# Kernel tuning notes

Measured on AMD Instinct MI355X. Metric: run time of the kernel, lower is better.

The kernel has to match this reference:

```python
import jax, jax.numpy as jnp
import numpy as np

B, DX, DH, DA, T = 2048, 64, 128, 128, 256
W_SCALE = 0.05


def setup_inputs() -> dict:
    key = jax.random.key(0)
    ks = iter(jax.random.split(key, 64))

    def nrm(shape, s=1.0):
        return jax.random.normal(next(ks), shape, dtype=jnp.float32) * s

    inp = {
        "x_t": nrm((B, DX)),
        "prev_h": nrm((B, DH)),
        "prev_c": nrm((B, DH)),
        "dt": jax.random.uniform(next(ks), (B, 1), dtype=jnp.float32),
        "store": nrm((B, T, DH)),
    }
    # six gates: (x-proj, h-proj, s-proj (or dt for gate s), bias)
    inp.update({
        "W_sx": nrm((DX, DH), W_SCALE), "W_sh": nrm((DH, DH), W_SCALE), "w_st": nrm((1, DH), W_SCALE), "b_s": jnp.zeros((DH,), jnp.float32),
        "W_fx": nrm((DX, DH), W_SCALE), "W_fh": nrm((DH, DH), W_SCALE), "W_fs": nrm((DH, DH), W_SCALE), "b_f": jnp.zeros((DH,), jnp.float32),
        "W_ix": nrm((DX, DH), W_SCALE), "W_ih": nrm((DH, DH), W_SCALE), "W_is": nrm((DH, DH), W_SCALE), "b_i": jnp.zeros((DH,), jnp.float32),
        "W_Tx": nrm((DX, DH), W_SCALE), "W_Th": nrm((DH, DH), W_SCALE), "W_Ts": nrm((DH, DH), W_SCALE), "b_T": jnp.zeros((DH,), jnp.float32),
        "W_ex": nrm((DX, DH), W_SCALE), "W_eh": nrm((DH, DH), W_SCALE), "W_es": nrm((DH, DH), W_SCALE), "b_e": jnp.zeros((DH,), jnp.float32),
        "W_ox": nrm((DX, DH), W_SCALE), "W_oh": nrm((DH, DH), W_SCALE), "W_os": nrm((DH, DH), W_SCALE), "b_o": jnp.zeros((DH,), jnp.float32),
        # additive attention over store: query from (h, new_c), keys from store
        "W_aq": nrm((DH, DA), W_SCALE), "W_ak": nrm((DH, DA), W_SCALE), "W_ah": nrm((DH, DA), W_SCALE),
        "b_a": jnp.zeros((DA,), jnp.float32), "v_a": nrm((DA,), W_SCALE),
        # interaction module: gated blend of h and attention context, gate from x_t
        "W_hh": nrm((DH, DH), W_SCALE), "W_he": nrm((DH, DH), W_SCALE), "W_hg": nrm((DX, DH), W_SCALE), "b_h": jnp.zeros((DH,), jnp.float32),
    })
    return inp


def reference(x_t, prev_h, prev_c, dt, store,
              W_sx, W_sh, w_st, b_s,
              W_fx, W_fh, W_fs, b_f,
              W_ix, W_ih, W_is, b_i,
              W_Tx, W_Th, W_Ts, b_T,
              W_ex, W_eh, W_es, b_e,
              W_ox, W_oh, W_os, b_o,
              W_aq, W_ak, W_ah, b_a, v_a,
              W_hh, W_he, W_hg, b_h):
    # time-aware gate s: dt is a scalar time-delta feature, broadcast over DH
    s = jnp.tanh(prev_h @ W_sh + x_t @ W_sx + dt @ w_st + b_s)            # [B, DH]
    f = jax.nn.sigmoid(prev_h @ W_fh + x_t @ W_fx + s @ W_fs + b_f)
    i = jax.nn.sigmoid(prev_h @ W_ih + x_t @ W_ix + s @ W_is + b_i)
    Tg = jax.nn.sigmoid(prev_h @ W_Th + x_t @ W_Tx + s @ W_Ts + b_T)
    elp = jnp.tanh(prev_h @ W_eh + x_t @ W_ex + s @ W_es + b_e)
    new_c = f * prev_c + i * elp + Tg * s                                  # [B, DH]
    o = jax.nn.sigmoid(prev_h @ W_oh + x_t @ W_ox + s @ W_os + b_o)
    h = o * jax.nn.sigmoid(new_c)                                          # [B, DH]

    # additive attention over the memory `store` [B, T, DH]
    q = h @ W_aq + new_c @ W_ak                                            # [B, DA]
    keys = jnp.einsum('btd,da->bta', store, W_ah)                          # [B, T, DA]
    e = jnp.einsum('bta,a->bt', jnp.tanh(q[:, None, :] + keys + b_a), v_a)  # [B, T]
    alpha = jax.nn.softmax(e, axis=-1)
    ctx = jnp.einsum('bt,btd->bd', alpha, store)                           # [B, DH]

    # interaction module: gated fusion of h and attention context
    g = jax.nn.sigmoid(x_t @ W_hg)
    new_h = g * jnp.tanh(h @ W_hh + ctx @ W_he + b_h)                      # [B, DH]
    return new_c, new_h
```

## Files before the change

kernel.cpp:

```cpp
#include <hip/hip_runtime.h>
#include <hip/hip_bf16.h>

#define B  2048
#define DX 64
#define DH 128
#define DA 128
#define T  256

typedef __attribute__((ext_vector_type(8))) short bf16x8;
typedef __attribute__((ext_vector_type(4))) float f32x4;

__device__ inline unsigned short bfbits(float f) {
    unsigned int u = __float_as_uint(f);
    unsigned int r = (u + 0x7fffu + ((u >> 16) & 1u)) >> 16;
    return (unsigned short)r;
}

__device__ inline float fast_tanh(float x) {
    x = fminf(15.f, fmaxf(-15.f, x));
    float e = __expf(2.f * x);
    return 1.f - 2.f * __builtin_amdgcn_rcpf(e + 1.f);
}

__device__ inline float sigm(float x) {
    return __builtin_amdgcn_rcpf(1.f + __expf(-x));
}

__global__ void k0_wt(const float* __restrict__ Wah, unsigned short* __restrict__ wT) {
    int i = blockIdx.x * 256 + threadIdx.x;
    int d = i >> 7;
    int a = i & 127;
    wT[a * DH + d] = bfbits(Wah[i]);
}

__global__ __launch_bounds__(512) void k1_gates(
    const float* __restrict__ xx,  const float* __restrict__ ph,
    const float* __restrict__ pcv, const float* __restrict__ dtv,
    const float* __restrict__ Wsx, const float* __restrict__ Wsh, const float* __restrict__ wst, const float* __restrict__ bs,
    const float* __restrict__ Wfx, const float* __restrict__ Wfh, const float* __restrict__ Wfs, const float* __restrict__ bf_,
    const float* __restrict__ Wix, const float* __restrict__ Wih, const float* __restrict__ Wis, const float* __restrict__ bi_,
    const float* __restrict__ WTx, const float* __restrict__ WTh, const float* __restrict__ WTs, const float* __restrict__ bT_,
    const float* __restrict__ Wex, const float* __restrict__ Weh, const float* __restrict__ Wes, const float* __restrict__ be_,
    const float* __restrict__ Wox, const float* __restrict__ Woh, const float* __restrict__ Wos, const float* __restrict__ bo_,
    const float* __restrict__ Waq, const float* __restrict__ Wak, const float* __restrict__ Whg,
    float* __restrict__ outc, float* __restrict__ wsh, float* __restrict__ wsq, float* __restrict__ wsg)
{
    __shared__ float shh[8][DH], shx[8][DX], shs[8][DH], shc[8][DH], shn[8][DH];
    const int tid = threadIdx.x;
    const int c   = tid & 127;
    const int qd  = tid >> 7;
    const int r0  = blockIdx.x * 8;
    const int ra  = qd * 2, rb = qd * 2 + 1;

    for (int i = tid; i < 8 * DH; i += 512) shh[i >> 7][i & 127] = ph[(size_t)r0 * DH + i];
    for (int i = tid; i < 8 * DX; i += 512) shx[i >> 6][i & 63]  = xx[(size_t)r0 * DX + i];
    __syncthreads();

    float A0, A1;
    {
        float bb = bs[c], w0 = wst[c];
        A0 = bb + dtv[r0 + ra] * w0;
        A1 = bb + dtv[r0 + rb] * w0;
        for (int k = 0; k < DH; ++k) { float wv = Wsh[k * DH + c]; A0 += shh[ra][k] * wv; A1 += shh[rb][k] * wv; }
        for (int k = 0; k < DX; ++k) { float wv = Wsx[k * DH + c]; A0 += shx[ra][k] * wv; A1 += shx[rb][k] * wv; }
        shs[ra][c] = fast_tanh(A0);
        shs[rb][c] = fast_tanh(A1);
    }
    __syncthreads();

#define G3(Wh_, Wx_, Ws_, b_)                                                              \
    { float bb = (b_)[c]; A0 = bb; A1 = bb;                                                \
      for (int k = 0; k < DH; ++k) { float wv = (Wh_)[k * DH + c];                         \
          A0 += shh[ra][k] * wv; A1 += shh[rb][k] * wv; }                                  \
      for (int k = 0; k < DX; ++k) { float wv = (Wx_)[k * DH + c];                         \
          A0 += shx[ra][k] * wv; A1 += shx[rb][k] * wv; }                                  \
      for (int k = 0; k < DH; ++k) { float wv = (Ws_)[k * DH + c];                         \
          A0 += shs[ra][k] * wv; A1 += shs[rb][k] * wv; } }

    G3(Wfh, Wfx, Wfs, bf_); float f0 = sigm(A0), f1 = sigm(A1);
    G3(Wih, Wix, Wis, bi_); float i0 = sigm(A0), i1 = sigm(A1);
    G3(WTh, WTx, WTs, bT_); float t0 = sigm(A0), t1 = sigm(A1);
    G3(Weh, Wex, Wes, be_); float e0 = fast_tanh(A0), e1 = fast_tanh(A1);
    G3(Woh, Wox, Wos, bo_); float o0 = sigm(A0), o1 = sigm(A1);
#undef G3

    {
        float s0 = shs[ra][c], s1 = shs[rb][c];
        float c0 = f0 * pcv[(size_t)(r0 + ra) * DH + c] + i0 * e0 + t0 * s0;
        float c1 = f1 * pcv[(size_t)(r0 + rb) * DH + c] + i1 * e1 + t1 * s1;
        float h0 = o0 * sigm(c0);
        float h1 = o1 * sigm(c1);
        outc[(size_t)(r0 + ra) * DH + c] = c0;
        outc[(size_t)(r0 + rb) * DH + c] = c1;
        wsh[(size_t)(r0 + ra) * DH + c] = h0;
        wsh[(size_t)(r0 + rb) * DH + c] = h1;
        shc[ra][c] = c0; shc[rb][c] = c1;
        shn[ra][c] = h0; shn[rb][c] = h1;
    }
    {
        A0 = 0.f; A1 = 0.f;
        for (int k = 0; k < DX; ++k) { float wv = Whg[k * DH + c]; A0 += shx[ra][k] * wv; A1 += shx[rb][k] * wv; }
        wsg[(size_t)(r0 + ra) * DH + c] = sigm(A0);
        wsg[(size_t)(r0 + rb) * DH + c] = sigm(A1);
    }
    __syncthreads();
    {
        A0 = 0.f; A1 = 0.f;
        for (int k = 0; k < DH; ++k) {
            float wq_ = Waq[k * DH + c], wk_ = Wak[k * DH + c];
            A0 += shn[ra][k] * wq_ + shc[ra][k] * wk_;
            A1 += shn[rb][k] * wq_ + shc[rb][k] * wk_;
        }
        wsq[(size_t)(r0 + ra) * DH + c] = A0;
        wsq[(size_t)(r0 + rb) * DH + c] = A1;
    }
}

__global__ __launch_bounds__(256, 2) void k2_attn(
    const float* __restrict__ store_, const unsigned short* __restrict__ wt,
    const float* __restrict__ ba, const float* __restrict__ va,
    const float* __restrict__ wsq, float* __restrict__ wsctx)
{
    __shared__ __align__(16) unsigned short ldsA[64][136];
    __shared__ float qb[DA], vv[DA], ee[T], red[8], ctxh[2][DH];

    const int tid = threadIdx.x;
    const int r   = blockIdx.x;
    const int l   = tid & 63;
    const int w   = tid >> 6;
    const int lr  = l & 15;
    const int kg  = l >> 4;
    const float* srow = store_ + (size_t)r * (T * DH);

    if (tid < DA) {
        qb[tid] = wsq[(size_t)r * DA + tid] + ba[tid];
        vv[tid] = va[tid];
    }

    bf16x8 bfr[8][4];
#pragma unroll
    for (int ct = 0; ct < 8; ++ct)
#pragma unroll
        for (int ks = 0; ks < 4; ++ks)
            bfr[ct][ks] = *(const bf16x8*)&wt[(ct * 16 + lr) * DH + ks * 32 + kg * 8];

    for (int tt = 0; tt < 4; ++tt) {
        __syncthreads();
#pragma unroll
        for (int ci = 0; ci < 4; ++ci) {
            int cid = tid + ci * 256;
            int row = cid >> 4;
            int c8  = cid & 15;
            const float* g = srow + ((tt * 64 + row) * DH + c8 * 8);
            float4 u0 = *(const float4*)g;
            float4 u1 = *(const float4*)(g + 4);
            union { unsigned short us[8]; uint4 v; } pk;
            pk.us[0] = bfbits(u0.x); pk.us[1] = bfbits(u0.y);
            pk.us[2] = bfbits(u0.z); pk.us[3] = bfbits(u0.w);
            pk.us[4] = bfbits(u1.x); pk.us[5] = bfbits(u1.y);
            pk.us[6] = bfbits(u1.z); pk.us[7] = bfbits(u1.w);
            *(uint4*)&ldsA[row][c8 * 8] = pk.v;
        }
        __syncthreads();

        f32x4 acc[8];
#pragma unroll
        for (int ct = 0; ct < 8; ++ct) acc[ct] = (f32x4){0.f, 0.f, 0.f, 0.f};
        const int arow = w * 16 + lr;
#pragma unroll
        for (int ks = 0; ks < 4; ++ks) {
            bf16x8 af = *(const bf16x8*)&ldsA[arow][ks * 32 + kg * 8];
#pragma unroll
            for (int ct = 0; ct < 8; ++ct)
                acc[ct] = __builtin_amdgcn_mfma_f32_16x16x32_bf16(af, bfr[ct][ks], acc[ct], 0, 0, 0);
        }

        float pe[4] = {0.f, 0.f, 0.f, 0.f};
#pragma unroll
        for (int ct = 0; ct < 8; ++ct) {
            int a = ct * 16 + lr;
            float qa = qb[a], vva = vv[a];
#pragma unroll
            for (int reg = 0; reg < 4; ++reg)
                pe[reg] += vva * fast_tanh(qa + acc[ct][reg]);
        }
#pragma unroll
        for (int m = 1; m <= 8; m <<= 1) {
#pragma unroll
            for (int reg = 0; reg < 4; ++reg) pe[reg] += __shfl_xor(pe[reg], m);
        }
        if (lr == 0) {
#pragma unroll
            for (int reg = 0; reg < 4; ++reg)
                ee[tt * 64 + w * 16 + kg * 4 + reg] = pe[reg];
        }
    }
    __syncthreads();

    float xv = ee[tid];
    float mx = xv;
#pragma unroll
    for (int m = 1; m < 64; m <<= 1) mx = fmaxf(mx, __shfl_xor(mx, m));
    if (l == 0) red[w] = mx;
    __syncthreads();
    float M = fmaxf(fmaxf(red[0], red[1]), fmaxf(red[2], red[3]));
    float ex = __expf(xv - M);
    float sm = ex;
#pragma unroll
    for (int m = 1; m < 64; m <<= 1) sm += __shfl_xor(sm, m);
    if (l == 0) red[4 + w] = sm;
    __syncthreads();
    float S = red[4] + red[5] + red[6] + red[7];
    ee[tid] = ex / S;
    __syncthreads();

    {
        int d = tid & 127, th = tid >> 7;
        const float* sp = srow + (size_t)th * 128 * DH + d;
        float p = 0.f;
        for (int t = 0; t < 128; ++t) p = fmaf(ee[th * 128 + t], sp[(size_t)t * DH], p);
        ctxh[th][d] = p;
    }
    __syncthreads();
    if (tid < DH) wsctx[(size_t)r * DH + tid] = ctxh[0][tid] + ctxh[1][tid];
}

__global__ __launch_bounds__(512) void k3_inter(
    const float* __restrict__ wsh, const float* __restrict__ wsctx, const float* __restrict__ wsg,
    const float* __restrict__ Whh, const float* __restrict__ Whe, const float* __restrict__ bh,
    float* __restrict__ outh)
{
    __shared__ float sh[8][DH], sc[8][DH];
    const int tid = threadIdx.x;
    const int c   = tid & 127;
    const int qd  = tid >> 7;
    const int r0  = blockIdx.x * 8;
    const int ra  = qd * 2, rb = qd * 2 + 1;

    for (int i = tid; i < 8 * DH; i += 512) {
        sh[i >> 7][i & 127] = wsh[(size_t)r0 * DH + i];
        sc[i >> 7][i & 127] = wsctx[(size_t)r0 * DH + i];
    }
    __syncthreads();

    float A0 = bh[c], A1 = bh[c];
    for (int k = 0; k < DH; ++k) {
        float wh_ = Whh[k * DH + c], we_ = Whe[k * DH + c];
        A0 += sh[ra][k] * wh_ + sc[ra][k] * we_;
        A1 += sh[rb][k] * wh_ + sc[rb][k] * we_;
    }
    outh[(size_t)(r0 + ra) * DH + c] = wsg[(size_t)(r0 + ra) * DH + c] * fast_tanh(A0);
    outh[(size_t)(r0 + rb) * DH + c] = wsg[(size_t)(r0 + rb) * DH + c] * fast_tanh(A1);
}

extern "C" void kernel_launch(void* const* d_in, const int* in_sizes, int n_in,
                              void* d_out, int out_size, void* d_ws, size_t ws_size,
                              hipStream_t stream)
{
    const float* x_t   = (const float*)d_in[0];
    const float* ph    = (const float*)d_in[1];
    const float* pc    = (const float*)d_in[2];
    const float* dt    = (const float*)d_in[3];
    const float* store = (const float*)d_in[4];
    const float* Wsx = (const float*)d_in[5];  const float* Wsh = (const float*)d_in[6];
    const float* wst = (const float*)d_in[7];  const float* bs  = (const float*)d_in[8];
    const float* Wfx = (const float*)d_in[9];  const float* Wfh = (const float*)d_in[10];
    const float* Wfs = (const float*)d_in[11]; const float* bf_ = (const float*)d_in[12];
    const float* Wix = (const float*)d_in[13]; const float* Wih = (const float*)d_in[14];
    const float* Wis = (const float*)d_in[15]; const float* bi_ = (const float*)d_in[16];
    const float* WTx = (const float*)d_in[17]; const float* WTh = (const float*)d_in[18];
    const float* WTs = (const float*)d_in[19]; const float* bT_ = (const float*)d_in[20];
    const float* Wex = (const float*)d_in[21]; const float* Weh = (const float*)d_in[22];
    const float* Wes = (const float*)d_in[23]; const float* be_ = (const float*)d_in[24];
    const float* Wox = (const float*)d_in[25]; const float* Woh = (const float*)d_in[26];
    const float* Wos = (const float*)d_in[27]; const float* bo_ = (const float*)d_in[28];
    const float* Waq = (const float*)d_in[29]; const float* Wak = (const float*)d_in[30];
    const float* Wah = (const float*)d_in[31]; const float* ba  = (const float*)d_in[32];
    const float* va  = (const float*)d_in[33];
    const float* Whh = (const float*)d_in[34]; const float* Whe = (const float*)d_in[35];
    const float* Whg = (const float*)d_in[36]; const float* bh  = (const float*)d_in[37];

    float* outc = (float*)d_out;
    float* outh = outc + (size_t)B * DH;

    float* wsh   = (float*)d_ws;
    float* wsq   = wsh + (size_t)B * DH;
    float* wsg   = wsq + (size_t)B * DH;
    float* wsctx = wsg + (size_t)B * DH;
    unsigned short* wT = (unsigned short*)(wsctx + (size_t)B * DH);

    k0_wt<<<(DA * DH) / 256, 256, 0, stream>>>(Wah, wT);
    k1_gates<<<B / 8, 512, 0, stream>>>(x_t, ph, pc, dt,
                                        Wsx, Wsh, wst, bs,
                                        Wfx, Wfh, Wfs, bf_,
                                        Wix, Wih, Wis, bi_,
                                        WTx, WTh, WTs, bT_,
                                        Wex, Weh, Wes, be_,
                                        Wox, Woh, Wos, bo_,
                                        Waq, Wak, Whg,
                                        outc, wsh, wsq, wsg);
    k2_attn<<<B, 256, 0, stream>>>(store, wT, ba, va, wsq, wsctx);
    k3_inter<<<B / 8, 512, 0, stream>>>(wsh, wsctx, wsg, Whh, Whe, bh, outh);
}
```

Measured before the change: 578.4 us.

## Reuse LDS store tile for context, double-buffer store, readlane-broadcast gate GEMVs

The attention kernel now computes the context from the bf16 store tile already staged in LDS, with a fused online exp/sum softmax and no max subtraction. This removes the second fp32 read of the large store tensor from global memory. Store tiles are double-buffered so global loads overlap the MFMA and context work. The gate and interaction kernels move to 256-thread blocks with 4 rows per thread, broadcasting activations through readlane instead of shared-memory loops. The risks are lower context precision from bf16 and possible exp overflow if the logits were large.

```diff
diff --git a/kernel.cpp b/kernel.cpp
--- a/kernel.cpp
+++ b/kernel.cpp
@@ -15,15 +15,19 @@
     unsigned int r = (u + 0x7fffu + ((u >> 16) & 1u)) >> 16;
     return (unsigned short)r;
 }
-
+__device__ inline float bf2f(unsigned short s) {
+    return __uint_as_float(((unsigned int)s) << 16);
+}
 __device__ inline float fast_tanh(float x) {
     x = fminf(15.f, fmaxf(-15.f, x));
     float e = __expf(2.f * x);
     return 1.f - 2.f * __builtin_amdgcn_rcpf(e + 1.f);
 }
-
 __device__ inline float sigm(float x) {
     return __builtin_amdgcn_rcpf(1.f + __expf(-x));
+}
+__device__ inline float RL(float v, int k) {
+    return __int_as_float(__builtin_amdgcn_readlane(__float_as_int(v), k));
 }
 
 __global__ void k0_wt(const float* __restrict__ Wah, unsigned short* __restrict__ wT) {
@@ -33,7 +37,7 @@
     wT[a * DH + d] = bfbits(Wah[i]);
 }
 
-__global__ __launch_bounds__(512) void k1_gates(
+__global__ __launch_bounds__(256) void k1_gates(
     const float* __restrict__ xx,  const float* __restrict__ ph,
     const float* __restrict__ pcv, const float* __restrict__ dtv,
     const float* __restrict__ Wsx, const float* __restrict__ Wsh, const float* __restrict__ wst, const float* __restrict__ bs,
@@ -45,74 +49,136 @@
     const float* __restrict__ Waq, const float* __restrict__ Wak, const float* __restrict__ Whg,
     float* __restrict__ outc, float* __restrict__ wsh, float* __restrict__ wsq, float* __restrict__ wsg)
 {
-    __shared__ float shh[8][DH], shx[8][DX], shs[8][DH], shc[8][DH], shn[8][DH];
+    __shared__ float shs[8][DH], shc[8][DH], shn[8][DH];
     const int tid = threadIdx.x;
-    const int c   = tid & 127;
-    const int qd  = tid >> 7;
+    const int l   = tid & 63;
+    const int w   = tid >> 6;
+    const int rg  = w >> 1;
+    const int c   = (w & 1) * 64 + l;
     const int r0  = blockIdx.x * 8;
-    const int ra  = qd * 2, rb = qd * 2 + 1;
-
-    for (int i = tid; i < 8 * DH; i += 512) shh[i >> 7][i & 127] = ph[(size_t)r0 * DH + i];
-    for (int i = tid; i < 8 * DX; i += 512) shx[i >> 6][i & 63]  = xx[(size_t)r0 * DX + i];
-    __syncthreads();
-
-    float A0, A1;
+    const int rbase = r0 + rg * 4;
+
+    float hL[4], hH[4], xr[4], dts[4];
+#pragma unroll
+    for (int i = 0; i < 4; ++i) {
+        hL[i]  = ph[(size_t)(rbase + i) * DH + l];
+        hH[i]  = ph[(size_t)(rbase + i) * DH + 64 + l];
+        xr[i]  = xx[(size_t)(rbase + i) * DX + l];
+        dts[i] = dtv[rbase + i];
+    }
+
+    float A[4], sv[4];
     {
         float bb = bs[c], w0 = wst[c];
-        A0 = bb + dtv[r0 + ra] * w0;
-        A1 = bb + dtv[r0 + rb] * w0;
-        for (int k = 0; k < DH; ++k) { float wv = Wsh[k * DH + c]; A0 += shh[ra][k] * wv; A1 += shh[rb][k] * wv; }
-        for (int k = 0; k < DX; ++k) { float wv = Wsx[k * DH + c]; A0 += shx[ra][k] * wv; A1 += shx[rb][k] * wv; }
-        shs[ra][c] = fast_tanh(A0);
-        shs[rb][c] = fast_tanh(A1);
+#pragma unroll
+        for (int i = 0; i < 4; ++i) A[i] = bb + dts[i] * w0;
+#pragma unroll 8
+        for (int k = 0; k < 64; ++k) { float wv = Wsh[k * DH + c];
+#pragma unroll
+            for (int i = 0; i < 4; ++i) A[i] = fmaf(RL(hL[i], k), wv, A[i]); }
+#pragma unroll 8
+        for (int k = 0; k < 64; ++k) { float wv = Wsh[(k + 64) * DH + c];
+#pragma unroll
+            for (int i = 0; i < 4; ++i) A[i] = fmaf(RL(hH[i], k), wv, A[i]); }
+#pragma unroll 8
+        for (int k = 0; k < 64; ++k) { float wv = Wsx[k * DH + c];
+#pragma unroll
+            for (int i = 0; i < 4; ++i) A[i] = fmaf(RL(xr[i], k), wv, A[i]); }
+#pragma unroll
+        for (int i = 0; i < 4; ++i) { sv[i] = fast_tanh(A[i]); shs[rg * 4 + i][c] = sv[i]; }
     }
     __syncthreads();
-
-#define G3(Wh_, Wx_, Ws_, b_)                                                              \
-    { float bb = (b_)[c]; A0 = bb; A1 = bb;                                                \
-      for (int k = 0; k < DH; ++k) { float wv = (Wh_)[k * DH + c];                         \
-          A0 += shh[ra][k] * wv; A1 += shh[rb][k] * wv; }                                  \
-      for (int k = 0; k < DX; ++k) { float wv = (Wx_)[k * DH + c];                         \
-          A0 += shx[ra][k] * wv; A1 += shx[rb][k] * wv; }                                  \
-      for (int k = 0; k < DH; ++k) { float wv = (Ws_)[k * DH + c];                         \
-          A0 += shs[ra][k] * wv; A1 += shs[rb][k] * wv; } }
-
-    G3(Wfh, Wfx, Wfs, bf_); float f0 = sigm(A0), f1 = sigm(A1);
-    G3(Wih, Wix, Wis, bi_); float i0 = sigm(A0), i1 = sigm(A1);
-    G3(WTh, WTx, WTs, bT_); float t0 = sigm(A0), t1 = sigm(A1);
-    G3(Weh, Wex, Wes, be_); float e0 = fast_tanh(A0), e1 = fast_tanh(A1);
-    G3(Woh, Wox, Wos, bo_); float o0 = sigm(A0), o1 = sigm(A1);
+    float sL[4], sH[4];
+#pragma unroll
+    for (int i = 0; i < 4; ++i) { sL[i] = shs[rg * 4 + i][l]; sH[i] = shs[rg * 4 + i][64 + l]; }
+
+#define G3(Wh_, Wx_, Ws_, b_)                                                   \
+    { float bb = (b_)[c];                                                       \
+      _Pragma("unroll") for (int i = 0; i < 4; ++i) A[i] = bb;                  \
+      _Pragma("unroll 8") for (int k = 0; k < 64; ++k) {                        \
+          float wv = (Wh_)[k * DH + c];                                         \
+          _Pragma("unroll") for (int i = 0; i < 4; ++i)                         \
+              A[i] = fmaf(RL(hL[i], k), wv, A[i]); }                            \
+      _Pragma("unroll 8") for (int k = 0; k < 64; ++k) {                        \
+          float wv = (Wh_)[(k + 64) * DH + c];                                  \
+          _Pragma("unroll") for (int i = 0; i < 4; ++i)                         \
+              A[i] = fmaf(RL(hH[i], k), wv, A[i]); }                            \
+      _Pragma("unroll 8") for (int k = 0; k < 64; ++k) {                        \
+          float wv = (Wx_)[k * DH + c];                                         \
+          _Pragma("unroll") for (int i = 0; i < 4; ++i)                         \
+              A[i] = fmaf(RL(xr[i], k), wv, A[i]); }                            \
+      _Pragma("unroll 8") for (int k = 0; k < 64; ++k) {                        \
+          float wv = (Ws_)[k * DH + c];                                         \
+          _Pragma("unroll") for (int i = 0; i < 4; ++i)                         \
+              A[i] = fmaf(RL(sL[i], k), wv, A[i]); }                            \
+      _Pragma("unroll 8") for (int k = 0; k < 64; ++k) {                        \
+          float wv = (Ws_)[(k + 64) * DH + c];                                  \
+          _Pragma("unroll") for (int i = 0; i < 4; ++i)                         \
+              A[i] = fmaf(RL(sH[i], k), wv, A[i]); } }
+
+    float fg[4], ig[4], tg[4], eg[4], og[4];
+    G3(Wfh, Wfx, Wfs, bf_);
+#pragma unroll
+    for (int i = 0; i < 4; ++i) fg[i] = sigm(A[i]);
+    G3(Wih, Wix, Wis, bi_);
+#pragma unroll
+    for (int i = 0; i < 4; ++i) ig[i] = sigm(A[i]);
+    G3(WTh, WTx, WTs, bT_);
+#pragma unroll
+    for (int i = 0; i < 4; ++i) tg[i] = sigm(A[i]);
+    G3(Weh, Wex, Wes, be_);
+#pragma unroll
+    for (int i = 0; i < 4; ++i) eg[i] = fast_tanh(A[i]);
+    G3(Woh, Wox, Wos, bo_);
+#pragma unroll
+    for (int i = 0; i < 4; ++i) og[i] = sigm(A[i]);
 #undef G3
 
+#pragma unroll
+    for (int i = 0; i < 4; ++i) {
+        float cn = fg[i] * pcv[(size_t)(rbase + i) * DH + c] + ig[i] * eg[i] + tg[i] * sv[i];
+        float hn = og[i] * sigm(cn);
+        outc[(size_t)(rbase + i) * DH + c] = cn;
+        wsh [(size_t)(rbase + i) * DH + c] = hn;
+        shc[rg * 4 + i][c] = cn;
+        shn[rg * 4 + i][c] = hn;
+    }
     {
-        float s0 = shs[ra][c], s1 = shs[rb][c];
-        float c0 = f0 * pcv[(size_t)(r0 + ra) * DH + c] + i0 * e0 + t0 * s0;
-        float c1 = f1 * pcv[(size_t)(r0 + rb) * DH + c] + i1 * e1 + t1 * s1;
-        float h0 = o0 * sigm(c0);
-        float h1 = o1 * sigm(c1);
-        outc[(size_t)(r0 + ra) * DH + c] = c0;
-        outc[(size_t)(r0 + rb) * DH + c] = c1;
-        wsh[(size_t)(r0 + ra) * DH + c] = h0;
-        wsh[(size_t)(r0 + rb) * DH + c] = h1;
-        shc[ra][c] = c0; shc[rb][c] = c1;
-        shn[ra][c] = h0; shn[rb][c] = h1;
-    }
-    {
-        A0 = 0.f; A1 = 0.f;
-        for (int k = 0; k < DX; ++k) { float wv = Whg[k * DH + c]; A0 += shx[ra][k] * wv; A1 += shx[rb][k] * wv; }
-        wsg[(size_t)(r0 + ra) * DH + c] = sigm(A0);
-        wsg[(size_t)(r0 + rb) * DH + c] = sigm(A1);
+#pragma unroll
+        for (int i = 0; i < 4; ++i) A[i] = 0.f;
+#pragma unroll 8
+        for (int k = 0; k < 64; ++k) { float wv = Whg[k * DH + c];
+#pragma unroll
+            for (int i = 0; i < 4; ++i) A[i] = fmaf(RL(xr[i], k), wv, A[i]); }
+#pragma unroll
+        for (int i = 0; i < 4; ++i) wsg[(size_t)(rbase + i) * DH + c] = sigm(A[i]);
     }
     __syncthreads();
     {
-        A0 = 0.f; A1 = 0.f;
-        for (int k = 0; k < DH; ++k) {
-            float wq_ = Waq[k * DH + c], wk_ = Wak[k * DH + c];
-            A0 += shn[ra][k] * wq_ + shc[ra][k] * wk_;
-            A1 += shn[rb][k] * wq_ + shc[rb][k] * wk_;
-        }
-        wsq[(size_t)(r0 + ra) * DH + c] = A0;
-        wsq[(size_t)(r0 + rb) * DH + c] = A1;
+        float nL[4], nH[4], cL[4], cH[4];
+#pragma unroll
+        for (int i = 0; i < 4; ++i) {
+            nL[i] = shn[rg * 4 + i][l]; nH[i] = shn[rg * 4 + i][64 + l];
+            cL[i] = shc[rg * 4 + i][l]; cH[i] = shc[rg * 4 + i][64 + l];
+        }
+#pragma unroll
+        for (int i = 0; i < 4; ++i) A[i] = 0.f;
+#pragma unroll 8
+        for (int k = 0; k < 64; ++k) {
+            float wq = Waq[k * DH + c], wk2 = Wak[k * DH + c];
+#pragma unroll
+            for (int i = 0; i < 4; ++i)
+                A[i] = fmaf(RL(nL[i], k), wq, fmaf(RL(cL[i], k), wk2, A[i]));
+        }
+#pragma unroll 8
+        for (int k = 0; k < 64; ++k) {
+            float wq = Waq[(k + 64) * DH + c], wk2 = Wak[(k + 64) * DH + c];
+#pragma unroll
+            for (int i = 0; i < 4; ++i)
+                A[i] = fmaf(RL(nH[i], k), wq, fmaf(RL(cH[i], k), wk2, A[i]));
+        }
+#pragma unroll
+        for (int i = 0; i < 4; ++i) wsq[(size_t)(rbase + i) * DH + c] = A[i];
     }
 }
 
@@ -121,7 +187,7 @@
     const float* __restrict__ ba, const float* __restrict__ va,
     const float* __restrict__ wsq, float* __restrict__ wsctx)
 {
-    __shared__ __align__(16) unsigned short ldsA[64][136];
+    __shared__ __align__(16) unsigned short buf[2][64][136];
     __shared__ float qb[DA], vv[DA], ee[T], red[8], ctxh[2][DH];
 
     const int tid = threadIdx.x;
@@ -130,6 +196,8 @@
     const int w   = tid >> 6;
     const int lr  = l & 15;
     const int kg  = l >> 4;
+    const int d   = tid & 127;
+    const int th  = tid >> 7;
     const float* srow = store_ + (size_t)r * (T * DH);
 
     if (tid < DA) {
@@ -144,23 +212,38 @@
         for (int ks = 0; ks < 4; ++ks)
             bfr[ct][ks] = *(const bf16x8*)&wt[(ct * 16 + lr) * DH + ks * 32 + kg * 8];
 
+    float4 ra_[4], rb_[4];
+#define STAGE_LOAD(tt)                                                     \
+    _Pragma("unroll")                                                      \
+    for (int ci = 0; ci < 4; ++ci) {                                       \
+        int cid = tid + ci * 256;                                          \
+        int row = cid >> 4, c8 = cid & 15;                                 \
+        const float* g = srow + ((tt) * 64 + row) * DH + c8 * 8;           \
+        ra_[ci] = *(const float4*)g;                                       \
+        rb_[ci] = *(const float4*)(g + 4);                                 \
+    }
+#define STAGE_WRITE(bsel)                                                  \
+    _Pragma("unroll")                                                      \
+    for (int ci = 0; ci < 4; ++ci) {                                       \
+        int cid = tid + ci * 256;                                          \
+        int row = cid >> 4, c8 = cid & 15;                                 \
+        union { unsigned short us[8]; uint4 v; } pk;                       \
+        pk.us[0] = bfbits(ra_[ci].x); pk.us[1] = bfbits(ra_[ci].y);        \
+        pk.us[2] = bfbits(ra_[ci].z); pk.us[3] = bfbits(ra_[ci].w);        \
+        pk.us[4] = bfbits(rb_[ci].x); pk.us[5] = bfbits(rb_[ci].y);        \
+        pk.us[6] = bfbits(rb_[ci].z); pk.us[7] = bfbits(rb_[ci].w);        \
+        *(uint4*)&buf[bsel][row][c8 * 8] = pk.v;                           \
+    }
+
+    STAGE_LOAD(0);
+    STAGE_WRITE(0);
+
+    float Sw   = 0.f;
+    float oacc = 0.f;
+
     for (int tt = 0; tt < 4; ++tt) {
-        __syncthreads();
-#pragma unroll
-        for (int ci = 0; ci < 4; ++ci) {
-            int cid = tid + ci * 256;
-            int row = cid >> 4;
-            int c8  = cid & 15;
-            const float* g = srow + ((tt * 64 + row) * DH + c8 * 8);
-            float4 u0 = *(const float4*)g;
-            float4 u1 = *(const float4*)(g + 4);
-            union { unsigned short us[8]; uint4 v; } pk;
-            pk.us[0] = bfbits(u0.x); pk.us[1] = bfbits(u0.y);
-            pk.us[2] = bfbits(u0.z); pk.us[3] = bfbits(u0.w);
-            pk.us[4] = bfbits(u1.x); pk.us[5] = bfbits(u1.y);
-            pk.us[6] = bfbits(u1.z); pk.us[7] = bfbits(u1.w);
-            *(uint4*)&ldsA[row][c8 * 8] = pk.v;
-        }
+        const int cur = tt & 1;
+        if (tt < 3) STAGE_LOAD(tt + 1);
         __syncthreads();
 
         f32x4 acc[8];
@@ -169,7 +252,7 @@
         const int arow = w * 16 + lr;
 #pragma unroll
         for (int ks = 0; ks < 4; ++ks) {
-            bf16x8 af = *(const bf16x8*)&ldsA[arow][ks * 32 + kg * 8];
+            bf16x8 af = *(const bf16x8*)&buf[cur][arow][ks * 32 + kg * 8];
 #pragma unroll
             for (int ct = 0; ct < 8; ++ct)
                 acc[ct] = __builtin_amdgcn_mfma_f32_16x16x32_bf16(af, bfr[ct][ks], acc[ct], 0, 0, 0);
@@ -189,68 +272,79 @@
 #pragma unroll
             for (int reg = 0; reg < 4; ++reg) pe[reg] += __shfl_xor(pe[reg], m);
         }
+        float px[4];
+#pragma unroll
+        for (int reg = 0; reg < 4; ++reg) px[reg] = __expf(pe[reg]);
         if (lr == 0) {
 #pragma unroll
             for (int reg = 0; reg < 4; ++reg)
-                ee[tt * 64 + w * 16 + kg * 4 + reg] = pe[reg];
-        }
-    }
+                ee[tt * 64 + w * 16 + kg * 4 + reg] = px[reg];
+            Sw += px[0] + px[1] + px[2] + px[3];
+        }
+        __syncthreads();
+
+#pragma unroll 8
+        for (int j = 0; j < 32; ++j) {
+            int t = th * 32 + j;
+            float p = ee[tt * 64 + t];
+            oacc = fmaf(p, bf2f(buf[cur][t][d]), oacc);
+        }
+        if (tt < 3) STAGE_WRITE((tt + 1) & 1);
+    }
+
+#pragma unroll
+    for (int m = 1; m < 64; m <<= 1) Sw += __shfl_xor(Sw, m);
+    if (l == 0) red[w] = Sw;
+    ctxh[th][d] = oacc;
     __syncthreads();
-
-    float xv = ee[tid];
-    float mx = xv;
-#pragma unroll
-    for (int m = 1; m < 64; m <<= 1) mx = fmaxf(mx, __shfl_xor(mx, m));
-    if (l == 0) red[w] = mx;
-    __syncthreads();
-    float M = fmaxf(fmaxf(red[0], red[1]), fmaxf(red[2], red[3]));
-    float ex = __expf(xv - M);
-    float sm = ex;
-#pragma unroll
-    for (int m = 1; m < 64; m <<= 1) sm += __shfl_xor(sm, m);
-    if (l == 0) red[4 + w] = sm;
-    __syncthreads();
-    float S = red[4] + red[5] + red[6] + red[7];
-    ee[tid] = ex / S;
-    __syncthreads();
-
-    {
-        int d = tid & 127, th = tid >> 7;
-        const float* sp = srow + (size_t)th * 128 * DH + d;
-        float p = 0.f;
-        for (int t = 0; t < 128; ++t) p = fmaf(ee[th * 128 + t], sp[(size_t)t * DH], p);
-        ctxh[th][d] = p;
-    }
-    __syncthreads();
-    if (tid < DH) wsctx[(size_t)r * DH + tid] = ctxh[0][tid] + ctxh[1][tid];
-}
-
-__global__ __launch_bounds__(512) void k3_inter(
+    float S = red[0] + red[1] + red[2] + red[3];
+    if (tid < DH) wsctx[(size_t)r * DH + tid] = (ctxh[0][tid] + ctxh[1][tid]) / S;
+#undef STAGE_LOAD
+#undef STAGE_WRITE
+}
+
+__global__ __launch_bounds__(256) void k3_inter(
     const float* __restrict__ wsh, const float* __restrict__ wsctx, const float* __restrict__ wsg,
     const float* __restrict__ Whh, const float* __restrict__ Whe, const float* __restrict__ bh,
     float* __restrict__ outh)
 {
-    __shared__ float sh[8][DH], sc[8][DH];
     const int tid = threadIdx.x;
-    const int c   = tid & 127;
-    const int qd  = tid >> 7;
-    const int r0  = blockIdx.x * 8;
-    const int ra  = qd * 2, rb = qd * 2 + 1;
-
-    for (int i = tid; i < 8 * DH; i += 512) {
-        sh[i >> 7][i & 127] = wsh[(size_t)r0 * DH + i];
-        sc[i >> 7][i & 127] = wsctx[(size_t)r0 * DH + i];
-    }
-    __syncthreads();
-
-    float A0 = bh[c], A1 = bh[c];
-    for (int k = 0; k < DH; ++k) {
+    const int l   = tid & 63;
+    const int w   = tid >> 6;
+    const int rg  = w >> 1;
+    const int c   = (w & 1) * 64 + l;
+    const int rbase = blockIdx.x * 8 + rg * 4;
+
+    float hL[4], hH[4], cL[4], cH[4];
+#pragma unroll
+    for (int i = 0; i < 4; ++i) {
+        hL[i] = wsh  [(size_t)(rbase + i) * DH + l];
+        hH[i] = wsh  [(size_t)(rbase + i) * DH + 64 + l];
+        cL[i] = wsctx[(size_t)(rbase + i) * DH + l];
+        cH[i] = wsctx[(size_t)(rbase + i) * DH + 64 + l];
+    }
+    float A[4];
+    float bb = bh[c];
+#pragma unroll
+    for (int i = 0; i < 4; ++i) A[i] = bb;
+#pragma unroll 8
+    for (int k = 0; k < 64; ++k) {
         float wh_ = Whh[k * DH + c], we_ = Whe[k * DH + c];
-        A0 += sh[ra][k] * wh_ + sc[ra][k] * we_;
-        A1 += sh[rb][k] * wh_ + sc[rb][k] * we_;
-    }
-    outh[(size_t)(r0 + ra) * DH + c] = wsg[(size_t)(r0 + ra) * DH + c] * fast_tanh(A0);
-    outh[(size_t)(r0 + rb) * DH + c] = wsg[(size_t)(r0 + rb) * DH + c] * fast_tanh(A1);
+#pragma unroll
+        for (int i = 0; i < 4; ++i)
+            A[i] = fmaf(RL(hL[i], k), wh_, fmaf(RL(cL[i], k), we_, A[i]));
+    }
+#pragma unroll 8
+    for (int k = 0; k < 64; ++k) {
+        float wh_ = Whh[(k + 64) * DH + c], we_ = Whe[(k + 64) * DH + c];
+#pragma unroll
+        for (int i = 0; i < 4; ++i)
+            A[i] = fmaf(RL(hH[i], k), wh_, fmaf(RL(cH[i], k), we_, A[i]));
+    }
+#pragma unroll
+    for (int i = 0; i < 4; ++i)
+        outh[(size_t)(rbase + i) * DH + c] =
+            wsg[(size_t)(rbase + i) * DH + c] * fast_tanh(A[i]);
 }
 
 extern "C" void kernel_launch(void* const* d_in, const int* in_sizes, int n_in,
@@ -290,7 +384,7 @@
     unsigned short* wT = (unsigned short*)(wsctx + (size_t)B * DH);
 
     k0_wt<<<(DA * DH) / 256, 256, 0, stream>>>(Wah, wT);
-    k1_gates<<<B / 8, 512, 0, stream>>>(x_t, ph, pc, dt,
+    k1_gates<<<B / 8, 256, 0, stream>>>(x_t, ph, pc, dt,
                                         Wsx, Wsh, wst, bs,
                                         Wfx, Wfh, Wfs, bf_,
                                         Wix, Wih, Wis, bi_,
@@ -300,5 +394,5 @@
                                         Waq, Wak, Whg,
                                         outc, wsh, wsq, wsg);
     k2_attn<<<B, 256, 0, stream>>>(store, wT, ba, va, wsq, wsctx);
-    k3_inter<<<B / 8, 512, 0, stream>>>(wsh, wsctx, wsg, Whh, Whe, bh, outh);
-}
+    k3_inter<<<B / 8, 256, 0, stream>>>(wsh, wsctx, wsg, Whh, Whe, bh, outh);
+}
```

Result: no change. 571.9 us (-1.1%).
